# Kernel tuning notes

Measured on AMD Instinct MI355X. Metric: run time of the kernel, lower is better.

## Reference

```python
import jax, jax.numpy as jnp
import numpy as np

B, V, N, IN_F, HEADS, OUT_F = 4, 4, 1000, 64, 4, 32
D = HEADS * OUT_F  # 128, concat=True
E = 64000
NEG_SLOPE = 0.2


def setup_inputs() -> dict:
    key = jax.random.key(0)
    ks = jax.random.split(key, 8)
    x = jax.random.normal(ks[0], (B, V, N, IN_F), jnp.float32)
    edge_index = jax.random.randint(ks[1], (2, E), 0, B * N, dtype=jnp.int64)
    W = jax.random.normal(ks[2], (HEADS * OUT_F, IN_F), jnp.float32) / np.sqrt(IN_F)
    att = jax.random.normal(ks[3], (1, HEADS, 2 * OUT_F), jnp.float32) * 0.1
    in_proj_w = jax.random.normal(ks[4], (3 * D, D), jnp.float32) / np.sqrt(D)
    in_proj_b = jnp.zeros((3 * D,), jnp.float32)
    out_proj_w = jax.random.normal(ks[5], (D, D), jnp.float32) / np.sqrt(D)
    out_proj_b = jnp.zeros((D,), jnp.float32)
    bias = jnp.zeros((D,), jnp.float32)
    return dict(x=x, W=W, att=att, in_proj_w=in_proj_w, in_proj_b=in_proj_b,
                out_proj_w=out_proj_w, out_proj_b=out_proj_b, bias=bias,
                edge_index=edge_index)


def reference(x, W, att, in_proj_w, in_proj_b, out_proj_w, out_proj_b, bias, edge_index):
    Bx, Vx, Nx, _ = x.shape
    Ntot = Bx * Nx
    # intra-view GAT: shared W across views
    h = jnp.einsum('bvni,oi->bvno', x, W).reshape(Bx, Vx, Nx, HEADS, OUT_F)
    # block-diagonal placement: h_full[b*V+v, b*N:(b+1)*N] = h[b,v]
    ib = jnp.arange(Bx)
    hf = jnp.zeros((Bx, Vx, Bx, Nx, HEADS, OUT_F), x.dtype).at[ib, :, ib].set(h)
    h_full = hf.reshape(Bx * Vx, Ntot, HEADS, OUT_F)
    # add self loops
    loops = jnp.arange(Ntot, dtype=edge_index.dtype)
    src = jnp.concatenate([edge_index[0], loops])
    dst = jnp.concatenate([edge_index[1], loops])
    # attention scores (faithful to source: flatten h_full over (B*V, Ntot) and
    # index with raw node ids, i.e. gathers from block 0 only)
    h_flat = h_full.reshape(Bx * Vx * Ntot, HEADS, OUT_F)
    h_cat = jnp.concatenate([h_flat[src], h_flat[dst]], axis=-1)  # [Etot, H, 2*OUT]
    att_in = jax.nn.leaky_relu(h_cat, NEG_SLOPE)
    scores = jnp.sum(att * att_in, axis=-1)  # [Etot, HEADS]
    # per-destination segment softmax
    seg_max = jax.ops.segment_max(scores, dst, num_segments=Ntot)
    seg_max = jax.lax.stop_gradient(jnp.where(jnp.isfinite(seg_max), seg_max, 0.0))
    ex = jnp.exp(scores - seg_max[dst])
    denom = jax.ops.segment_sum(ex, dst, num_segments=Ntot)
    alpha = ex / (denom[dst] + 1e-16)  # [Etot, HEADS]
    # scatter-add aggregation, broadcast over B*V rows
    msgs = h_full[:, src] * alpha[None, :, :, None]  # [B*V, Etot, H, OUT]
    out_full = jnp.zeros_like(h_full).at[:, dst].add(msgs)
    # extract each graph's own node block
    out = out_full.reshape(Bx, Vx, Bx, Nx, HEADS, OUT_F)[ib, :, ib]  # [B,V,N,H,OUT]
    h_gat = out.reshape(Bx, Vx, Nx, HEADS * OUT_F)  # concat heads
    # inter-view mixing: MHA over the V axis per node
    seq = h_gat.transpose(0, 2, 1, 3).reshape(Bx * Nx, Vx, D)
    q, k, v = jnp.split(seq @ in_proj_w.T + in_proj_b, 3, axis=-1)
    hd = D // HEADS
    sp = lambda t: t.reshape(Bx * Nx, Vx, HEADS, hd).transpose(0, 2, 1, 3)
    q, k, v = sp(q), sp(k), sp(v)
    aw = jax.nn.softmax(jnp.einsum('bhqd,bhkd->bhqk', q, k) / jnp.sqrt(jnp.asarray(hd, x.dtype)), axis=-1)
    ao = jnp.einsum('bhqk,bhkd->bhqd', aw, v).transpose(0, 2, 1, 3).reshape(Bx * Nx, Vx, D)
    mixed = ao @ out_proj_w.T + out_proj_b
    h_mixed = mixed.reshape(Bx, Nx, Vx, D).transpose(0, 2, 1, 3)  # [B,V,N,D]
    return h_mixed + bias
```

## Files before the change

kernel.cpp:

```cpp
#include <hip/hip_runtime.h>

#define NN 1000
#define HEADS_ 4
#define DM 128
#define EE 64000
#define NTOT 4000
#define ETOT 68000
#define CAP 48
#define EB 34

template <int K, int SCORE>
__device__ void gemm_tile(int mi, int ni,
                          const float* __restrict__ A, const float* __restrict__ Wt,
                          float* __restrict__ C, int N,
                          const float* __restrict__ att,
                          float* __restrict__ ssrc, float* __restrict__ sdst) {
  __shared__ float As[128 * 64];
  __shared__ float Bs[64 * 64];
  int tid = threadIdx.x;
  int m0 = mi * 128, n0 = ni * 64;
  int tx = tid & 15, ty = tid >> 4;
  const float4* A4 = (const float4*)A;
  const float4* W4 = (const float4*)Wt;
  float acc[8][4] = {};

  for (int c = 0; c < K / 64; ++c) {
    __syncthreads();
    {
      int q = tid & 15;
      int r0 = tid >> 4;
#pragma unroll
      for (int p = 0; p < 8; ++p) {
        int r = r0 + p * 16;
        float4 v = A4[(size_t)(m0 + r) * (K / 4) + c * 16 + q];
        *(float4*)&As[r * 64 + ((q ^ ((r >> 2) & 15)) << 2)] = v;
      }
#pragma unroll
      for (int p = 0; p < 4; ++p) {
        int r = r0 + p * 16;
        float4 v = W4[(size_t)(n0 + r) * (K / 4) + c * 16 + q];
        *(float4*)&Bs[r * 64 + ((q ^ ((r >> 2) & 15)) << 2)] = v;
      }
    }
    __syncthreads();
#pragma unroll 4
    for (int q = 0; q < 16; ++q) {
      float4 a[8], b[4];
#pragma unroll
      for (int i = 0; i < 8; ++i) {
        int r = ty * 8 + i;
        a[i] = *(const float4*)&As[r * 64 + ((q ^ ((r >> 2) & 15)) << 2)];
      }
#pragma unroll
      for (int j = 0; j < 4; ++j) {
        int rn = tx * 4 + j;
        b[j] = *(const float4*)&Bs[rn * 64 + ((q ^ ((rn >> 2) & 15)) << 2)];
      }
#pragma unroll
      for (int i = 0; i < 8; ++i)
#pragma unroll
        for (int j = 0; j < 4; ++j)
          acc[i][j] += a[i].x * b[j].x + a[i].y * b[j].y
                     + a[i].z * b[j].z + a[i].w * b[j].w;
    }
  }

  int nc = n0 + tx * 4;
#pragma unroll
  for (int i = 0; i < 8; ++i) {
    int m = m0 + ty * 8 + i;
    float4 o = make_float4(acc[i][0], acc[i][1], acc[i][2], acc[i][3]);
    *(float4*)&C[(size_t)m * N + nc] = o;
  }

  if (SCORE && m0 < NN) {
    int hsel = tx >> 3;
    int h = ni * 2 + hsel;
    int kb = (tx & 7) * 4;
    float a0[4], a1[4];
#pragma unroll
    for (int j = 0; j < 4; ++j) {
      a0[j] = att[h * 64 + kb + j];
      a1[j] = att[h * 64 + 32 + kb + j];
    }
#pragma unroll
    for (int i = 0; i < 8; ++i) {
      int m = m0 + ty * 8 + i;
      float p0 = 0.f, p1 = 0.f;
#pragma unroll
      for (int j = 0; j < 4; ++j) {
        float g = acc[i][j];
        float lr = g > 0.f ? g : 0.2f * g;
        p0 += a0[j] * lr;
        p1 += a1[j] * lr;
      }
      p0 += __shfl_xor(p0, 1, 16); p1 += __shfl_xor(p1, 1, 16);
      p0 += __shfl_xor(p0, 2, 16); p1 += __shfl_xor(p1, 2, 16);
      p0 += __shfl_xor(p0, 4, 16); p1 += __shfl_xor(p1, 4, 16);
      if ((tx & 7) == 0 && m < NN) {
        ssrc[m * HEADS_ + h] = p0;
        sdst[m * HEADS_ + h] = p1;
      }
    }
  }
}

__global__ __launch_bounds__(256) void k1_kernel(const float* __restrict__ x,
                                                 const float* __restrict__ W,
                                                 const float* __restrict__ att,
                                                 float* __restrict__ hbuf,
                                                 float* __restrict__ ssrc,
                                                 float* __restrict__ sdst,
                                                 const int* __restrict__ ei,
                                                 int* __restrict__ cnt,
                                                 int* __restrict__ elist) {
  int bid = blockIdx.x;
  if (bid < 250) {
    gemm_tile<64, 1>(bid >> 1, bid & 1, x, W, hbuf, 128, att, ssrc, sdst);
  } else {
    for (int e = (bid - 250) * 256 + threadIdx.x; e < ETOT; e += EB * 256) {
      int s, d;
      if (e < EE) { s = ei[e]; d = ei[EE + e]; }
      else { s = d = e - EE; }
      int pos = atomicAdd(&cnt[d], 1);
      if (pos < CAP) elist[d * CAP + pos] = s;
    }
  }
}

__global__ __launch_bounds__(256) void gather_kernel(const int* __restrict__ cnt,
                                                     const int* __restrict__ elist,
                                                     const float* __restrict__ ssrc,
                                                     const float* __restrict__ sdst,
                                                     const float* __restrict__ hbuf,
                                                     float* __restrict__ hgat) {
  __shared__ int   srcs[2][CAP];
  __shared__ float exs[2][CAP][HEADS_];
  int li = threadIdx.x >> 7;
  int t = threadIdx.x & 127;
  int d = blockIdx.x * 2 + li;
  int b = d / NN;
  int v = t >> 5, q = t & 31, h = q >> 3;
  int m = cnt[d]; if (m > CAP) m = CAP;
  for (int base = 0; base < m; base += 32) {
    int i = base + (t >> 2);
    if (i < m) {
      int s = elist[d * CAP + i];
      if ((t & 3) == 0) srcs[li][i] = s;
      float sc = ssrc[s * HEADS_ + (t & 3)] + sdst[d * HEADS_ + (t & 3)];
      exs[li][i][t & 3] = __expf(sc);
    }
  }
  __syncthreads();
  float den = 1e-16f;
  float4 acc = make_float4(0.f, 0.f, 0.f, 0.f);
  const float* hbase = hbuf + ((size_t)(b * 4 + v) * NN) * DM + q * 4;
  for (int i = 0; i < m; ++i) {
    float ex = exs[li][i][h];
    den += ex;
    unsigned sl = (unsigned)(srcs[li][i] - b * NN);
    if (sl < NN) {
      float4 hv = *(const float4*)(hbase + (size_t)sl * DM);
      acc.x += ex * hv.x; acc.y += ex * hv.y;
      acc.z += ex * hv.z; acc.w += ex * hv.w;
    }
  }
  float r = 1.f / den;
  acc.x *= r; acc.y *= r; acc.z *= r; acc.w *= r;
  *(float4*)&hgat[((size_t)(d * 4 + v)) * DM + q * 4] = acc;
}

#define QS 388

__global__ __launch_bounds__(256) void fused3_kernel(const float* __restrict__ hgat,
                                                     const float* __restrict__ inw,
                                                     const float* __restrict__ inb,
                                                     const float* __restrict__ outw,
                                                     const float* __restrict__ outb,
                                                     const float* __restrict__ bias,
                                                     float* __restrict__ out) {
  extern __shared__ float smem[];
  float* As = smem;
  float* Bs = smem + 8192;
  float* qk = smem + 12288;
  float* aw = smem + 37120;

  int tid = threadIdx.x;
  int g0 = blockIdx.x * 16;
  int tx = tid & 15, ty = tid >> 4;

  {
    const float4* H4 = (const float4*)(hgat + (size_t)(g0 * 4) * DM);
#pragma unroll
    for (int p = 0; p < 8; ++p) {
      int idx = p * 256 + tid;
      int r = idx >> 5, qp = idx & 31;
      float4 v = H4[idx];
      int c = qp >> 4, q = qp & 15;
      *(float4*)&As[c * 4096 + r * 64 + ((q ^ ((r >> 2) & 15)) << 2)] = v;
    }
  }

  const float4* W4 = (const float4*)inw;
  for (int ni = 0; ni < 6; ++ni) {
    float acc[4][4] = {};
    for (int c = 0; c < 2; ++c) {
      __syncthreads();
      {
        int q = tid & 15, r0 = tid >> 4;
#pragma unroll
        for (int p = 0; p < 4; ++p) {
          int r = r0 + p * 16;
          float4 v = W4[(size_t)(ni * 64 + r) * 32 + c * 16 + q];
          *(float4*)&Bs[r * 64 + ((q ^ ((r >> 2) & 15)) << 2)] = v;
        }
      }
      __syncthreads();
#pragma unroll 4
      for (int q = 0; q < 16; ++q) {
        float4 a[4], b[4];
#pragma unroll
        for (int i = 0; i < 4; ++i) {
          int r = ty * 4 + i;
          a[i] = *(const float4*)&As[c * 4096 + r * 64 + ((q ^ ((r >> 2) & 15)) << 2)];
        }
#pragma unroll
        for (int j = 0; j < 4; ++j) {
          int rn = tx * 4 + j;
          b[j] = *(const float4*)&Bs[rn * 64 + ((q ^ ((rn >> 2) & 15)) << 2)];
        }
#pragma unroll
        for (int i = 0; i < 4; ++i)
#pragma unroll
          for (int j = 0; j < 4; ++j)
            acc[i][j] += a[i].x * b[j].x + a[i].y * b[j].y
                       + a[i].z * b[j].z + a[i].w * b[j].w;
      }
    }
    int nc = ni * 64 + tx * 4;
    float b0 = inb[nc], b1 = inb[nc + 1], b2 = inb[nc + 2], b3 = inb[nc + 3];
#pragma unroll
    for (int i = 0; i < 4; ++i) {
      int r = ty * 4 + i;
      *(float4*)&qk[r * QS + nc] =
          make_float4(acc[i][0] + b0, acc[i][1] + b1, acc[i][2] + b2, acc[i][3] + b3);
    }
  }
  __syncthreads();

  {
    int ln = tid >> 4, vq = (tid >> 2) & 3, h = tid & 3;
    float4 qv[8];
    const float* qr = &qk[(ln * 4 + vq) * QS + h * 32];
#pragma unroll
    for (int u = 0; u < 8; ++u) qv[u] = *(const float4*)&qr[u * 4];
    float sc[4];
#pragma unroll
    for (int vk = 0; vk < 4; ++vk) {
      const float* kr = &qk[(ln * 4 + vk) * QS + 128 + h * 32];
      float s = 0.f;
#pragma unroll
      for (int u = 0; u < 8; ++u) {
        float4 kv = *(const float4*)&kr[u * 4];
        s += qv[u].x * kv.x + qv[u].y * kv.y + qv[u].z * kv.z + qv[u].w * kv.w;
      }
      sc[vk] = s * 0.17677669529663687f;
    }
    float mx = fmaxf(fmaxf(sc[0], sc[1]), fmaxf(sc[2], sc[3]));
    float e0 = __expf(sc[0] - mx), e1 = __expf(sc[1] - mx);
    float e2 = __expf(sc[2] - mx), e3 = __expf(sc[3] - mx);
    float inv = 1.f / (e0 + e1 + e2 + e3);
    aw[tid * 4 + 0] = e0 * inv; aw[tid * 4 + 1] = e1 * inv;
    aw[tid * 4 + 2] = e2 * inv; aw[tid * 4 + 3] = e3 * inv;
  }
  __syncthreads();

  {
    int ln = tid >> 4, rem = tid & 15, vq = rem >> 2, h = rem & 3;
    float wv[4];
#pragma unroll
    for (int vk = 0; vk < 4; ++vk)
      wv[vk] = aw[((ln << 4) + (vq << 2) + h) * 4 + vk];
    int r = ln * 4 + vq;
#pragma unroll
    for (int u = 0; u < 8; ++u) {
      float4 a4 = make_float4(0.f, 0.f, 0.f, 0.f);
#pragma unroll
      for (int vk = 0; vk < 4; ++vk) {
        float4 vv = *(const float4*)&qk[(ln * 4 + vk) * QS + 256 + h * 32 + u * 4];
        a4.x += wv[vk] * vv.x; a4.y += wv[vk] * vv.y;
        a4.z += wv[vk] * vv.z; a4.w += wv[vk] * vv.w;
      }
      int qp = h * 8 + u, c = qp >> 4, q = qp & 15;
      *(float4*)&As[c * 4096 + r * 64 + ((q ^ ((r >> 2) & 15)) << 2)] = a4;
    }
  }

  const float4* O4 = (const float4*)outw;
  for (int ni = 0; ni < 2; ++ni) {
    float acc[4][4] = {};
    for (int c = 0; c < 2; ++c) {
      __syncthreads();
      {
        int q = tid & 15, r0 = tid >> 4;
#pragma unroll
        for (int p = 0; p < 4; ++p) {
          int r = r0 + p * 16;
          float4 v = O4[(size_t)(ni * 64 + r) * 32 + c * 16 + q];
          *(float4*)&Bs[r * 64 + ((q ^ ((r >> 2) & 15)) << 2)] = v;
        }
      }
      __syncthreads();
#pragma unroll 4
      for (int q = 0; q < 16; ++q) {
        float4 a[4], b[4];
#pragma unroll
        for (int i = 0; i < 4; ++i) {
          int r = ty * 4 + i;
          a[i] = *(const float4*)&As[c * 4096 + r * 64 + ((q ^ ((r >> 2) & 15)) << 2)];
        }
#pragma unroll
        for (int j = 0; j < 4; ++j) {
          int rn = tx * 4 + j;
          b[j] = *(const float4*)&Bs[rn * 64 + ((q ^ ((rn >> 2) & 15)) << 2)];
        }
#pragma unroll
        for (int i = 0; i < 4; ++i)
#pragma unroll
          for (int j = 0; j < 4; ++j)
            acc[i][j] += a[i].x * b[j].x + a[i].y * b[j].y
                       + a[i].z * b[j].z + a[i].w * b[j].w;
      }
    }
    int nc = ni * 64 + tx * 4;
    float b0 = outb[nc] + bias[nc], b1 = outb[nc + 1] + bias[nc + 1];
    float b2 = outb[nc + 2] + bias[nc + 2], b3 = outb[nc + 3] + bias[nc + 3];
#pragma unroll
    for (int i = 0; i < 4; ++i) {
      int r = ty * 4 + i;
      int g = g0 + (r >> 2), v = r & 3;
      int bg = g / NN, n = g - bg * NN;
      int om = (bg * 4 + v) * NN + n;
      *(float4*)&out[(size_t)om * DM + nc] =
          make_float4(acc[i][0] + b0, acc[i][1] + b1, acc[i][2] + b2, acc[i][3] + b3);
    }
  }
}

extern "C" void kernel_launch(void* const* d_in, const int* in_sizes, int n_in,
                              void* d_out, int out_size, void* d_ws, size_t ws_size,
                              hipStream_t stream) {
  const float* x    = (const float*)d_in[0];
  const float* W    = (const float*)d_in[1];
  const float* att  = (const float*)d_in[2];
  const float* inw  = (const float*)d_in[3];
  const float* inb  = (const float*)d_in[4];
  const float* outw = (const float*)d_in[5];
  const float* outb = (const float*)d_in[6];
  const float* bias = (const float*)d_in[7];
  const int*   ei   = (const int*)d_in[8];
  float* out = (float*)d_out;

  float* ws = (float*)d_ws;
  float* hbuf  = ws;
  float* hgat  = ws + 2100000;
  float* ssrc  = ws + 12500000;
  float* sdst  = ssrc + 16000;
  int*   cnt   = (int*)(sdst + 16000);
  int*   elist = cnt + 4000;

  static int lds_opt_in = 0;
  if (!lds_opt_in) {
    hipFuncSetAttribute((const void*)fused3_kernel,
                        hipFuncAttributeMaxDynamicSharedMemorySize, 160 * 1024);
    lds_opt_in = 1;
  }

  hipMemsetAsync(ssrc, 0, 36000 * sizeof(float), stream);

  k1_kernel<<<250 + EB, 256, 0, stream>>>(x, W, att, hbuf, ssrc, sdst, ei, cnt, elist);
  gather_kernel<<<NTOT / 2, 256, 0, stream>>>(cnt, elist, ssrc, sdst, hbuf, hgat);
  fused3_kernel<<<250, 256, 152576, stream>>>(hgat, inw, inb, outw, outb, bias, out);
}
```

Measured before the change: 162.4 us.

## Restructure fused MHA kernel to 512 threads with 128-wide N tiles

Doubles the fused inter-view MHA block to 512 threads. The QKV projection now runs as three 128-column tiles held in registers across both K chunks, with the A tile streamed per chunk instead of preloaded. The attention step splits each head's dot product across two lanes combined with a shuffle, and the softmax weights stay in registers instead of going through shared memory. The output projection covers all 128 columns in a single pass. This is meant to raise parallelism within the 250 blocks and cut barriers and shared-memory traffic, at the cost of higher register pressure, since each thread holds 48 accumulators.

```diff
diff --git a/kernel.cpp b/kernel.cpp
--- a/kernel.cpp
+++ b/kernel.cpp
@@ -172,7 +172,7 @@
 
 #define QS 388
 
-__global__ __launch_bounds__(256) void fused3_kernel(const float* __restrict__ hgat,
+__global__ __launch_bounds__(512) void fused3_kernel(const float* __restrict__ hgat,
                                                      const float* __restrict__ inw,
                                                      const float* __restrict__ inb,
                                                      const float* __restrict__ outw,
@@ -181,37 +181,37 @@
                                                      float* __restrict__ out) {
   extern __shared__ float smem[];
   float* As = smem;
-  float* Bs = smem + 8192;
+  float* Bs = smem + 4096;
   float* qk = smem + 12288;
-  float* aw = smem + 37120;
+  float* ao = qk;
 
   int tid = threadIdx.x;
   int g0 = blockIdx.x * 16;
-  int tx = tid & 15, ty = tid >> 4;
-
-  {
-    const float4* H4 = (const float4*)(hgat + (size_t)(g0 * 4) * DM);
-#pragma unroll
-    for (int p = 0; p < 8; ++p) {
-      int idx = p * 256 + tid;
-      int r = idx >> 5, qp = idx & 31;
-      float4 v = H4[idx];
-      int c = qp >> 4, q = qp & 15;
-      *(float4*)&As[c * 4096 + r * 64 + ((q ^ ((r >> 2) & 15)) << 2)] = v;
-    }
-  }
-
+  int tx = tid & 31, ty = tid >> 5;
+
+  const float4* H4 = (const float4*)(hgat + (size_t)(g0 * 4) * DM);
   const float4* W4 = (const float4*)inw;
-  for (int ni = 0; ni < 6; ++ni) {
-    float acc[4][4] = {};
-    for (int c = 0; c < 2; ++c) {
+
+  float acc[3][4][4] = {};
+#pragma unroll
+  for (int c = 0; c < 2; ++c) {
+#pragma unroll
+    for (int ni = 0; ni < 3; ++ni) {
       __syncthreads();
       {
         int q = tid & 15, r0 = tid >> 4;
+        if (ni == 0) {
+#pragma unroll
+          for (int p = 0; p < 2; ++p) {
+            int r = r0 + p * 32;
+            float4 v = H4[r * 32 + c * 16 + q];
+            *(float4*)&As[r * 64 + ((q ^ ((r >> 2) & 15)) << 2)] = v;
+          }
+        }
 #pragma unroll
         for (int p = 0; p < 4; ++p) {
-          int r = r0 + p * 16;
-          float4 v = W4[(size_t)(ni * 64 + r) * 32 + c * 16 + q];
+          int r = r0 + p * 32;
+          float4 v = W4[(size_t)(ni * 128 + r) * 32 + c * 16 + q];
           *(float4*)&Bs[r * 64 + ((q ^ ((r >> 2) & 15)) << 2)] = v;
         }
       }
@@ -219,130 +219,142 @@
 #pragma unroll 4
       for (int q = 0; q < 16; ++q) {
         float4 a[4], b[4];
-#pragma unroll
-        for (int i = 0; i < 4; ++i) {
-          int r = ty * 4 + i;
-          a[i] = *(const float4*)&As[c * 4096 + r * 64 + ((q ^ ((r >> 2) & 15)) << 2)];
-        }
-#pragma unroll
-        for (int j = 0; j < 4; ++j) {
-          int rn = tx * 4 + j;
-          b[j] = *(const float4*)&Bs[rn * 64 + ((q ^ ((rn >> 2) & 15)) << 2)];
-        }
+        int sa = (q ^ ty) << 2;
+        int sb = (q ^ (tx & 15)) << 2;
 #pragma unroll
         for (int i = 0; i < 4; ++i)
+          a[i] = *(const float4*)&As[(ty * 4 + i) * 64 + sa];
+#pragma unroll
+        for (int j = 0; j < 4; ++j)
+          b[j] = *(const float4*)&Bs[(tx * 4 + j) * 64 + sb];
+#pragma unroll
+        for (int i = 0; i < 4; ++i)
 #pragma unroll
           for (int j = 0; j < 4; ++j)
-            acc[i][j] += a[i].x * b[j].x + a[i].y * b[j].y
-                       + a[i].z * b[j].z + a[i].w * b[j].w;
-      }
-    }
-    int nc = ni * 64 + tx * 4;
-    float b0 = inb[nc], b1 = inb[nc + 1], b2 = inb[nc + 2], b3 = inb[nc + 3];
+            acc[ni][i][j] += a[i].x * b[j].x + a[i].y * b[j].y
+                           + a[i].z * b[j].z + a[i].w * b[j].w;
+      }
+    }
+  }
+
+#pragma unroll
+  for (int ni = 0; ni < 3; ++ni) {
+    int nc = ni * 128 + tx * 4;
+    float4 bb = *(const float4*)&inb[nc];
 #pragma unroll
     for (int i = 0; i < 4; ++i) {
       int r = ty * 4 + i;
       *(float4*)&qk[r * QS + nc] =
-          make_float4(acc[i][0] + b0, acc[i][1] + b1, acc[i][2] + b2, acc[i][3] + b3);
+          make_float4(acc[ni][i][0] + bb.x, acc[ni][i][1] + bb.y,
+                      acc[ni][i][2] + bb.z, acc[ni][i][3] + bb.w);
     }
   }
   __syncthreads();
 
+  int ln = tid >> 5;
+  int vq2 = (tid >> 3) & 3, h2 = (tid >> 1) & 3, s2 = tid & 1;
+  float aww[4];
   {
-    int ln = tid >> 4, vq = (tid >> 2) & 3, h = tid & 3;
-    float4 qv[8];
-    const float* qr = &qk[(ln * 4 + vq) * QS + h * 32];
-#pragma unroll
-    for (int u = 0; u < 8; ++u) qv[u] = *(const float4*)&qr[u * 4];
+    const float* qr = &qk[(ln * 4 + vq2) * QS + h2 * 32 + s2 * 16];
+    float4 qv[4];
+#pragma unroll
+    for (int u = 0; u < 4; ++u) qv[u] = *(const float4*)&qr[u * 4];
     float sc[4];
 #pragma unroll
     for (int vk = 0; vk < 4; ++vk) {
-      const float* kr = &qk[(ln * 4 + vk) * QS + 128 + h * 32];
+      const float* kr = &qk[(ln * 4 + vk) * QS + 128 + h2 * 32 + s2 * 16];
       float s = 0.f;
 #pragma unroll
-      for (int u = 0; u < 8; ++u) {
+      for (int u = 0; u < 4; ++u) {
         float4 kv = *(const float4*)&kr[u * 4];
         s += qv[u].x * kv.x + qv[u].y * kv.y + qv[u].z * kv.z + qv[u].w * kv.w;
       }
-      sc[vk] = s * 0.17677669529663687f;
-    }
+      sc[vk] = s;
+    }
+#pragma unroll
+    for (int vk = 0; vk < 4; ++vk)
+      sc[vk] = (sc[vk] + __shfl_xor(sc[vk], 1)) * 0.17677669529663687f;
     float mx = fmaxf(fmaxf(sc[0], sc[1]), fmaxf(sc[2], sc[3]));
     float e0 = __expf(sc[0] - mx), e1 = __expf(sc[1] - mx);
     float e2 = __expf(sc[2] - mx), e3 = __expf(sc[3] - mx);
     float inv = 1.f / (e0 + e1 + e2 + e3);
-    aw[tid * 4 + 0] = e0 * inv; aw[tid * 4 + 1] = e1 * inv;
-    aw[tid * 4 + 2] = e2 * inv; aw[tid * 4 + 3] = e3 * inv;
+    aww[0] = e0 * inv; aww[1] = e1 * inv; aww[2] = e2 * inv; aww[3] = e3 * inv;
+  }
+
+  float4 o[4];
+#pragma unroll
+  for (int u = 0; u < 4; ++u) o[u] = make_float4(0.f, 0.f, 0.f, 0.f);
+#pragma unroll
+  for (int vk = 0; vk < 4; ++vk) {
+    const float* vr = &qk[(ln * 4 + vk) * QS + 256 + h2 * 32 + s2 * 16];
+    float w = aww[vk];
+#pragma unroll
+    for (int u = 0; u < 4; ++u) {
+      float4 vv = *(const float4*)&vr[u * 4];
+      o[u].x += w * vv.x; o[u].y += w * vv.y;
+      o[u].z += w * vv.z; o[u].w += w * vv.w;
+    }
   }
   __syncthreads();
-
   {
-    int ln = tid >> 4, rem = tid & 15, vq = rem >> 2, h = rem & 3;
-    float wv[4];
-#pragma unroll
-    for (int vk = 0; vk < 4; ++vk)
-      wv[vk] = aw[((ln << 4) + (vq << 2) + h) * 4 + vk];
-    int r = ln * 4 + vq;
-#pragma unroll
-    for (int u = 0; u < 8; ++u) {
-      float4 a4 = make_float4(0.f, 0.f, 0.f, 0.f);
-#pragma unroll
-      for (int vk = 0; vk < 4; ++vk) {
-        float4 vv = *(const float4*)&qk[(ln * 4 + vk) * QS + 256 + h * 32 + u * 4];
-        a4.x += wv[vk] * vv.x; a4.y += wv[vk] * vv.y;
-        a4.z += wv[vk] * vv.z; a4.w += wv[vk] * vv.w;
-      }
-      int qp = h * 8 + u, c = qp >> 4, q = qp & 15;
-      *(float4*)&As[c * 4096 + r * 64 + ((q ^ ((r >> 2) & 15)) << 2)] = a4;
-    }
-  }
-
+    int r = ln * 4 + vq2;
+#pragma unroll
+    for (int u = 0; u < 4; ++u) {
+      int qp = h2 * 8 + s2 * 4 + u;
+      int cc = qp >> 4, qg = qp & 15;
+      *(float4*)&ao[cc * 4096 + r * 64 + ((qg ^ (ln & 15)) << 2)] = o[u];
+    }
+  }
+  __syncthreads();
+
+  float oc[4][4] = {};
   const float4* O4 = (const float4*)outw;
-  for (int ni = 0; ni < 2; ++ni) {
-    float acc[4][4] = {};
-    for (int c = 0; c < 2; ++c) {
-      __syncthreads();
-      {
-        int q = tid & 15, r0 = tid >> 4;
-#pragma unroll
-        for (int p = 0; p < 4; ++p) {
-          int r = r0 + p * 16;
-          float4 v = O4[(size_t)(ni * 64 + r) * 32 + c * 16 + q];
-          *(float4*)&Bs[r * 64 + ((q ^ ((r >> 2) & 15)) << 2)] = v;
-        }
-      }
-      __syncthreads();
+#pragma unroll
+  for (int c = 0; c < 2; ++c) {
+    {
+      int q = tid & 15, r0 = tid >> 4;
+#pragma unroll
+      for (int p = 0; p < 4; ++p) {
+        int r = r0 + p * 32;
+        float4 v = O4[(size_t)r * 32 + c * 16 + q];
+        *(float4*)&Bs[r * 64 + ((q ^ ((r >> 2) & 15)) << 2)] = v;
+      }
+    }
+    __syncthreads();
 #pragma unroll 4
-      for (int q = 0; q < 16; ++q) {
-        float4 a[4], b[4];
-#pragma unroll
-        for (int i = 0; i < 4; ++i) {
-          int r = ty * 4 + i;
-          a[i] = *(const float4*)&As[c * 4096 + r * 64 + ((q ^ ((r >> 2) & 15)) << 2)];
-        }
-#pragma unroll
-        for (int j = 0; j < 4; ++j) {
-          int rn = tx * 4 + j;
-          b[j] = *(const float4*)&Bs[rn * 64 + ((q ^ ((rn >> 2) & 15)) << 2)];
-        }
-#pragma unroll
-        for (int i = 0; i < 4; ++i)
-#pragma unroll
-          for (int j = 0; j < 4; ++j)
-            acc[i][j] += a[i].x * b[j].x + a[i].y * b[j].y
-                       + a[i].z * b[j].z + a[i].w * b[j].w;
-      }
-    }
-    int nc = ni * 64 + tx * 4;
-    float b0 = outb[nc] + bias[nc], b1 = outb[nc + 1] + bias[nc + 1];
-    float b2 = outb[nc + 2] + bias[nc + 2], b3 = outb[nc + 3] + bias[nc + 3];
+    for (int q = 0; q < 16; ++q) {
+      float4 a[4], b[4];
+      int sa = (q ^ ty) << 2;
+      int sb = (q ^ (tx & 15)) << 2;
+#pragma unroll
+      for (int i = 0; i < 4; ++i)
+        a[i] = *(const float4*)&ao[c * 4096 + (ty * 4 + i) * 64 + sa];
+#pragma unroll
+      for (int j = 0; j < 4; ++j)
+        b[j] = *(const float4*)&Bs[(tx * 4 + j) * 64 + sb];
+#pragma unroll
+      for (int i = 0; i < 4; ++i)
+#pragma unroll
+        for (int j = 0; j < 4; ++j)
+          oc[i][j] += a[i].x * b[j].x + a[i].y * b[j].y
+                    + a[i].z * b[j].z + a[i].w * b[j].w;
+    }
+    __syncthreads();
+  }
+
+  {
+    int nc = tx * 4;
+    float4 ob = make_float4(outb[nc] + bias[nc], outb[nc + 1] + bias[nc + 1],
+                            outb[nc + 2] + bias[nc + 2], outb[nc + 3] + bias[nc + 3]);
 #pragma unroll
     for (int i = 0; i < 4; ++i) {
       int r = ty * 4 + i;
-      int g = g0 + (r >> 2), v = r & 3;
-      int bg = g / NN, n = g - bg * NN;
+      int node = g0 + (r >> 2), v = r & 3;
+      int bg = node / NN, n = node - bg * NN;
       int om = (bg * 4 + v) * NN + n;
       *(float4*)&out[(size_t)om * DM + nc] =
-          make_float4(acc[i][0] + b0, acc[i][1] + b1, acc[i][2] + b2, acc[i][3] + b3);
+          make_float4(oc[i][0] + ob.x, oc[i][1] + ob.y,
+                      oc[i][2] + ob.z, oc[i][3] + ob.w);
     }
   }
 }
@@ -380,5 +392,5 @@
 
   k1_kernel<<<250 + EB, 256, 0, stream>>>(x, W, att, hbuf, ssrc, sdst, ei, cnt, elist);
   gather_kernel<<<NTOT / 2, 256, 0, stream>>>(cnt, elist, ssrc, sdst, hbuf, hgat);
-  fused3_kernel<<<250, 256, 152576, stream>>>(hgat, inw, inb, outw, outb, bias, out);
-}
+  fused3_kernel<<<250, 512, 148480, stream>>>(hgat, inw, inb, outw, outb, bias, out);
+}
```

Result: faster. 144.4 us (-11.1%).
